# Performance work log

Hardware: AMD Instinct MI355X
Metric: run time of the kernel (lower is better)

The kernel has to match this reference:

```python
import jax, jax.numpy as jnp
import numpy as np

B, F, H, K, E = 512, 1280, 2560, 8, 9  # batch, feat_dim, 2*feat_dim, branching, n_internal
# Tree: root=node 0 (expert 0); level-1 nodes 1..8 (experts 1..8); level-2 leaves 9..72.

def setup_inputs() -> dict:
    key = jax.random.key(0)
    k0, k1, k2, k3, k4 = jax.random.split(key, 5)
    x = jax.random.normal(k0, (B, F), dtype=jnp.float32)
    W1 = jax.random.normal(k1, (E, F, H), dtype=jnp.float32) / np.sqrt(F)
    b1 = jnp.zeros((E, H), dtype=jnp.float32)
    W2 = jax.random.normal(k2, (E, H, K), dtype=jnp.float32) / np.sqrt(H)
    b2 = jnp.zeros((E, K), dtype=jnp.float32)
    return {"x": x, "W1": W1, "b1": b1, "W2": W2, "b2": b2}

def reference(x, W1, b1, W2, b2):
    # Batched experts: Linear(F->H) -> ReLU -> Linear(H->K), softmax over children.
    h = jax.nn.relu(jnp.einsum('bf,efh->ebh', x, W1) + b1[:, None, :])  # [E,B,H]
    logits = jnp.einsum('ebh,ehk->ebk', h, W2) + b2[:, None, :]          # [E,B,K]
    probs = jax.nn.softmax(logits, axis=-1)                              # [E,B,K]
    # Path products root->node for every node (matches leaf_probs in torch code).
    p0 = jnp.ones((1, x.shape[0]), dtype=x.dtype)        # root: prob 1        [1,B]
    p1 = probs[0].T                                       # nodes 1..8          [K,B]
    # leaves 9..72: parent of node n is 1+(n-9)//K, child index (n-9)%K
    p2 = (p1[:, None, :] * jnp.transpose(probs[1:E], (0, 2, 1))).reshape(K * K, -1)  # [64,B]
    leaf_probs = jnp.concatenate([p0, p1, p2], axis=0).T  # [B, 73]
    return leaf_probs, logits
```

## Files before the change

kernel.cpp:

```cpp
#include <hip/hip_runtime.h>

#define TB 512
#define TF 1280
#define TH 2560
#define TK 8
#define TE 9

typedef unsigned short ushortT;
typedef __attribute__((ext_vector_type(8))) short short8;
typedef __attribute__((ext_vector_type(4))) float floatx4;

__device__ __forceinline__ unsigned short f2bf(float f) {
  union { float f; unsigned u; } v; v.f = f;
  unsigned r = v.u + 0x7fffu + ((v.u >> 16) & 1u);
  return (unsigned short)(r >> 16);
}

__device__ __forceinline__ unsigned pk2(float a, float b) {
  union { float f; unsigned u; } ua, ub; ua.f = a; ub.f = b;
  unsigned ra = ua.u + 0x7fffu + ((ua.u >> 16) & 1u);
  unsigned rb = ub.u + 0x7fffu + ((ub.u >> 16) & 1u);
  return __builtin_amdgcn_perm(rb, ra, 0x07060302);
}

__device__ __forceinline__ void gl_lds16(const void* g, void* l) {
  __builtin_amdgcn_global_load_lds(
      (const __attribute__((address_space(1))) unsigned*)g,
      (__attribute__((address_space(3))) unsigned*)l, 16, 0, 0);
}

__global__ __launch_bounds__(256) void prepass(
    const float* __restrict__ x, const float* __restrict__ W2,
    ushortT* __restrict__ xb, ushortT* __restrict__ W2t) {
  const int i = blockIdx.x * 256 + threadIdx.x;
  if (i < TB * TF / 2) {
    float2 v = ((const float2*)x)[i];
    ((unsigned*)xb)[i] = pk2(v.x, v.y);
  } else {
    const int o = i - TB * TF / 2;
    if (o < TE * TK * TH) {
      const int hcol = o % TH;
      const int rest = o / TH;
      const int n = rest & 7;
      const int e = rest >> 3;
      W2t[(long)(e * TK + n) * TH + hcol] = f2bf(W2[((long)e * TH + hcol) * TK + n]);
    }
  }
}

__global__ __launch_bounds__(256, 3) void gemm1_relu(
    const ushortT* __restrict__ xb, const float* __restrict__ W1,
    const float* __restrict__ b1, ushortT* __restrict__ h) {
  __shared__ __align__(16) ushortT As[128 * 64];
  __shared__ __align__(16) ushortT Bs[128 * 72];

  const int t = threadIdx.x;
  const int tileN = blockIdx.x;
  const int e = tileN / 20;
  const int hbase = (tileN % 20) * 128;
  const int m0 = blockIdx.y * 128;

  const int lane = t & 63, w = t >> 6;
  const int wm = w & 1, wn = w >> 1;
  const int lm = lane & 15, lq = lane >> 4;

  const int kk4 = (t & 15) * 4;
  const int n0 = (t >> 4) * 8;

  floatx4 acc[4][4];
#pragma unroll
  for (int i = 0; i < 4; ++i)
#pragma unroll
    for (int j = 0; j < 4; ++j) acc[i][j] = (floatx4){0.f, 0.f, 0.f, 0.f};

  const float* wbase = W1 + ((long)e * TF) * TH + hbase + n0;

  floatx4 bv[4][2];
#pragma unroll
  for (int r = 0; r < 4; ++r)
#pragma unroll
    for (int c = 0; c < 2; ++c)
      bv[r][c] = *(const floatx4*)(wbase + (long)(kk4 + r) * TH + c * 4);

  for (int kt = 0; kt < TF / 64; ++kt) {
    const int k0 = kt * 64;
    if (kt) __syncthreads();

#pragma unroll
    for (int j = 0; j < 4; ++j) {
      const int s = j * 256 + w * 64 + lane;
      const int m = s >> 3;
      const int cc = (s & 7) ^ (m & 7);
      const ushortT* src = xb + (long)(m0 + m) * TF + k0 + cc * 8;
      gl_lds16(src, (void*)&As[(j * 256 + w * 64) * 8]);
    }
#pragma unroll
    for (int j = 0; j < 8; ++j) {
      const int c = j >> 2, q = j & 3;
      unsigned w0 = pk2(bv[0][c][q], bv[1][c][q]);
      unsigned w1 = pk2(bv[2][c][q], bv[3][c][q]);
      unsigned long long p = (unsigned long long)w0 | ((unsigned long long)w1 << 32);
      *(unsigned long long*)&Bs[(n0 + j) * 72 + kk4] = p;
    }
    __syncthreads();

    if (kt + 1 < TF / 64) {
#pragma unroll
      for (int r = 0; r < 4; ++r)
#pragma unroll
        for (int c = 0; c < 2; ++c)
          bv[r][c] = *(const floatx4*)(wbase + (long)(k0 + 64 + kk4 + r) * TH + c * 4);
    }

#pragma unroll
    for (int kk = 0; kk < 2; ++kk) {
      short8 af[4], bf[4];
#pragma unroll
      for (int mg = 0; mg < 4; ++mg) {
        const int m = wm * 64 + mg * 16 + lm;
        const int swz = (kk * 4 + lq) ^ (m & 7);
        af[mg] = *(const short8*)&As[m * 64 + swz * 8];
      }
#pragma unroll
      for (int ng = 0; ng < 4; ++ng) {
        const int n = wn * 64 + ng * 16 + lm;
        bf[ng] = *(const short8*)&Bs[n * 72 + kk * 32 + lq * 8];
      }
#pragma unroll
      for (int mg = 0; mg < 4; ++mg)
#pragma unroll
        for (int ng = 0; ng < 4; ++ng)
          acc[mg][ng] = __builtin_amdgcn_mfma_f32_16x16x32_bf16(af[mg], bf[ng], acc[mg][ng], 0, 0, 0);
    }
  }

#pragma unroll
  for (int mg = 0; mg < 4; ++mg) {
    const int row = m0 + wm * 64 + mg * 16 + lq * 4;
#pragma unroll
    for (int ng = 0; ng < 4; ++ng) {
      const int col = hbase + wn * 64 + ng * 16 + lm;
      const float bias = b1[e * TH + col];
      floatx4 c = acc[mg][ng];
#pragma unroll
      for (int r = 0; r < 4; ++r) {
        float v = c[r] + bias;
        v = v > 0.f ? v : 0.f;
        h[((long)e * TB + row + r) * TH + col] = f2bf(v);
      }
    }
  }
}

__global__ __launch_bounds__(256) void gemm2_softmax(
    const ushortT* __restrict__ h, const ushortT* __restrict__ W2t,
    const float* __restrict__ b2, float* __restrict__ logits_out,
    float* __restrict__ probs) {
  __shared__ float Ls[4][16][8];
  const int t = threadIdx.x;
  const int lane = t & 63, w = t >> 6;
  const int e = blockIdx.x >> 5;
  const int r0 = (blockIdx.x & 31) * 16;
  const int lm = lane & 15, lq = lane >> 4;

  const ushortT* hp = h + ((long)(e * TB + r0 + lm)) * TH + w * 640 + lq * 8;
  const int bn = lm < 8 ? lm : 7;
  const ushortT* wp = W2t + ((long)(e * TK + bn)) * TH + w * 640 + lq * 8;

  floatx4 acc = (floatx4){0.f, 0.f, 0.f, 0.f};
#pragma unroll
  for (int kt = 0; kt < 20; ++kt) {
    short8 a = *(const short8*)(hp + kt * 32);
    short8 b = *(const short8*)(wp + kt * 32);
    acc = __builtin_amdgcn_mfma_f32_16x16x32_bf16(a, b, acc, 0, 0, 0);
  }
  if (lm < 8) {
#pragma unroll
    for (int r = 0; r < 4; ++r) Ls[w][lq * 4 + r][lm] = acc[r];
  }
  __syncthreads();
  if (w == 0 && lm < 8) {
    const float bias = b2[e * TK + lm];
#pragma unroll
    for (int r = 0; r < 4; ++r) {
      const int row = lq * 4 + r;
      float v = Ls[0][row][lm] + Ls[1][row][lm] + Ls[2][row][lm] + Ls[3][row][lm] + bias;
      float mx = v;
      mx = fmaxf(mx, __shfl_xor(mx, 1, 64));
      mx = fmaxf(mx, __shfl_xor(mx, 2, 64));
      mx = fmaxf(mx, __shfl_xor(mx, 4, 64));
      float ex = __expf(v - mx);
      float sm = ex;
      sm += __shfl_xor(sm, 1, 64);
      sm += __shfl_xor(sm, 2, 64);
      sm += __shfl_xor(sm, 4, 64);
      const long idx = ((long)e * TB + r0 + row) * TK + lm;
      logits_out[idx] = v;
      probs[idx] = ex / sm;
    }
  }
}

__global__ __launch_bounds__(256) void leafk(const float* __restrict__ probs,
                                             float* __restrict__ out) {
  const int idx = blockIdx.x * 256 + threadIdx.x;
  if (idx >= TB * 73) return;
  const int b = idx / 73, c = idx % 73;
  float v;
  if (c == 0) {
    v = 1.0f;
  } else if (c < 9) {
    v = probs[(long)b * TK + (c - 1)];
  } else {
    const int i = (c - 9) >> 3, j = (c - 9) & 7;
    v = probs[(long)b * TK + i] * probs[((long)(1 + i) * TB + b) * TK + j];
  }
  out[idx] = v;
}

extern "C" void kernel_launch(void* const* d_in, const int* in_sizes, int n_in,
                              void* d_out, int out_size, void* d_ws, size_t ws_size,
                              hipStream_t stream) {
  const float* x  = (const float*)d_in[0];
  const float* W1 = (const float*)d_in[1];
  const float* b1 = (const float*)d_in[2];
  const float* W2 = (const float*)d_in[3];
  const float* b2 = (const float*)d_in[4];
  float* out = (float*)d_out;

  ushortT* h      = (ushortT*)d_ws;
  float*   probs  = (float*)((char*)d_ws + 23592960);
  ushortT* xb     = (ushortT*)((char*)d_ws + 23740416);
  ushortT* W2t    = (ushortT*)((char*)d_ws + 25051136);
  float* logits_out = out + TB * 73;

  prepass<<<2000, 256, 0, stream>>>(x, W2, xb, W2t);
  gemm1_relu<<<dim3(180, 4), 256, 0, stream>>>(xb, W1, b1, h);
  gemm2_softmax<<<TE * 32, 256, 0, stream>>>(h, W2t, b2, logits_out, probs);
  leafk<<<(TB * 73 + 255) / 256, 256, 0, stream>>>(probs, out);
}
```

Baseline: 245.2 us.

## Double-buffer W1 tile in LDS, load A fragments directly from global, remap grid

Rewrites the gemm1 main loop into a two-stage software pipeline, with two LDS buffers for the converted W1 tile and two register sets for the fp32 W1 prefetch. The x tile no longer goes through LDS: each wave loads its bf16 A fragments from global memory straight into registers, one k-step ahead. The grid becomes 1D with the four M tiles that share a W1 column tile placed on adjacent blocks, which should improve L2 reuse of W1, and launch bounds drop to 2 blocks per SM. The aim is fewer barriers and better overlap of global loads with MFMA, at the cost of higher register pressure, lower occupancy and uncoalesced, redundant global reads of A.

```diff
diff --git a/kernel.cpp b/kernel.cpp
--- a/kernel.cpp
+++ b/kernel.cpp
@@ -21,12 +21,6 @@
   unsigned ra = ua.u + 0x7fffu + ((ua.u >> 16) & 1u);
   unsigned rb = ub.u + 0x7fffu + ((ub.u >> 16) & 1u);
   return __builtin_amdgcn_perm(rb, ra, 0x07060302);
-}
-
-__device__ __forceinline__ void gl_lds16(const void* g, void* l) {
-  __builtin_amdgcn_global_load_lds(
-      (const __attribute__((address_space(1))) unsigned*)g,
-      (__attribute__((address_space(3))) unsigned*)l, 16, 0, 0);
 }
 
 __global__ __launch_bounds__(256) void prepass(
@@ -48,17 +42,18 @@
   }
 }
 
-__global__ __launch_bounds__(256, 3) void gemm1_relu(
+__global__ __launch_bounds__(256, 2) void gemm1_relu(
     const ushortT* __restrict__ xb, const float* __restrict__ W1,
     const float* __restrict__ b1, ushortT* __restrict__ h) {
-  __shared__ __align__(16) ushortT As[128 * 64];
-  __shared__ __align__(16) ushortT Bs[128 * 72];
+  __shared__ __align__(16) ushortT Bs[2][128 * 72];
 
   const int t = threadIdx.x;
-  const int tileN = blockIdx.x;
-  const int e = tileN / 20;
-  const int hbase = (tileN % 20) * 128;
-  const int m0 = blockIdx.y * 128;
+  const int bid = blockIdx.x;
+  const int ctile = bid >> 2;
+  const int mt = bid & 3;
+  const int e = ctile / 20;
+  const int hbase = (ctile % 20) * 128;
+  const int m0 = mt * 128;
 
   const int lane = t & 63, w = t >> 6;
   const int wm = w & 1, wn = w >> 1;
@@ -67,72 +62,82 @@
   const int kk4 = (t & 15) * 4;
   const int n0 = (t >> 4) * 8;
 
+  const float* wbase = W1 + ((long)e * TF) * TH + hbase + n0;
+  const ushortT* abase = xb + (long)(m0 + wm * 64 + lm) * TF + lq * 8;
+
   floatx4 acc[4][4];
 #pragma unroll
   for (int i = 0; i < 4; ++i)
 #pragma unroll
     for (int j = 0; j < 4; ++j) acc[i][j] = (floatx4){0.f, 0.f, 0.f, 0.f};
 
-  const float* wbase = W1 + ((long)e * TF) * TH + hbase + n0;
-
-  floatx4 bv[4][2];
-#pragma unroll
-  for (int r = 0; r < 4; ++r)
-#pragma unroll
-    for (int c = 0; c < 2; ++c)
-      bv[r][c] = *(const floatx4*)(wbase + (long)(kk4 + r) * TH + c * 4);
-
-  for (int kt = 0; kt < TF / 64; ++kt) {
-    const int k0 = kt * 64;
-    if (kt) __syncthreads();
-
-#pragma unroll
-    for (int j = 0; j < 4; ++j) {
-      const int s = j * 256 + w * 64 + lane;
-      const int m = s >> 3;
-      const int cc = (s & 7) ^ (m & 7);
-      const ushortT* src = xb + (long)(m0 + m) * TF + k0 + cc * 8;
-      gl_lds16(src, (void*)&As[(j * 256 + w * 64) * 8]);
-    }
+  floatx4 bva[4][2], bvb[4][2];
+  short8 afc[4][2], afn[4][2];
+
+  auto ldB = [&](floatx4 (&bv)[4][2], int kt) {
+    const float* p = wbase + (long)(kt * 64 + kk4) * TH;
+#pragma unroll
+    for (int r = 0; r < 4; ++r)
+#pragma unroll
+      for (int c = 0; c < 2; ++c)
+        bv[r][c] = *(const floatx4*)(p + (long)r * TH + c * 4);
+  };
+  auto wrB = [&](floatx4 (&bv)[4][2], int buf) {
 #pragma unroll
     for (int j = 0; j < 8; ++j) {
       const int c = j >> 2, q = j & 3;
       unsigned w0 = pk2(bv[0][c][q], bv[1][c][q]);
       unsigned w1 = pk2(bv[2][c][q], bv[3][c][q]);
       unsigned long long p = (unsigned long long)w0 | ((unsigned long long)w1 << 32);
-      *(unsigned long long*)&Bs[(n0 + j) * 72 + kk4] = p;
-    }
+      *(unsigned long long*)&Bs[buf][(n0 + j) * 72 + kk4] = p;
+    }
+  };
+  auto ldA = [&](short8 (&af)[4][2], int kt) {
+#pragma unroll
+    for (int mg = 0; mg < 4; ++mg)
+#pragma unroll
+      for (int kk = 0; kk < 2; ++kk)
+        af[mg][kk] = *(const short8*)(abase + (long)mg * 16 * TF + kt * 64 + kk * 32);
+  };
+  auto mma = [&](short8 (&af)[4][2], int buf) {
+#pragma unroll
+    for (int kk = 0; kk < 2; ++kk) {
+      short8 bf[4];
+#pragma unroll
+      for (int ng = 0; ng < 4; ++ng)
+        bf[ng] = *(const short8*)&Bs[buf][(wn * 64 + ng * 16 + lm) * 72 + kk * 32 + lq * 8];
+#pragma unroll
+      for (int mg = 0; mg < 4; ++mg)
+#pragma unroll
+        for (int ng = 0; ng < 4; ++ng)
+          acc[mg][ng] = __builtin_amdgcn_mfma_f32_16x16x32_bf16(af[mg][kk], bf[ng], acc[mg][ng], 0, 0, 0);
+    }
+  };
+
+  ldB(bva, 0);
+  ldB(bvb, 1);
+  ldA(afc, 0);
+  wrB(bva, 0);
+  __syncthreads();
+
+  for (int kt2 = 0; kt2 < 9; ++kt2) {
+    const int kt = 2 * kt2;
+    wrB(bvb, 1);
+    ldB(bva, kt + 2);
+    ldA(afn, kt + 1);
+    mma(afc, 0);
     __syncthreads();
-
-    if (kt + 1 < TF / 64) {
-#pragma unroll
-      for (int r = 0; r < 4; ++r)
-#pragma unroll
-        for (int c = 0; c < 2; ++c)
-          bv[r][c] = *(const floatx4*)(wbase + (long)(k0 + 64 + kk4 + r) * TH + c * 4);
-    }
-
-#pragma unroll
-    for (int kk = 0; kk < 2; ++kk) {
-      short8 af[4], bf[4];
-#pragma unroll
-      for (int mg = 0; mg < 4; ++mg) {
-        const int m = wm * 64 + mg * 16 + lm;
-        const int swz = (kk * 4 + lq) ^ (m & 7);
-        af[mg] = *(const short8*)&As[m * 64 + swz * 8];
-      }
-#pragma unroll
-      for (int ng = 0; ng < 4; ++ng) {
-        const int n = wn * 64 + ng * 16 + lm;
-        bf[ng] = *(const short8*)&Bs[n * 72 + kk * 32 + lq * 8];
-      }
-#pragma unroll
-      for (int mg = 0; mg < 4; ++mg)
-#pragma unroll
-        for (int ng = 0; ng < 4; ++ng)
-          acc[mg][ng] = __builtin_amdgcn_mfma_f32_16x16x32_bf16(af[mg], bf[ng], acc[mg][ng], 0, 0, 0);
-    }
-  }
+    wrB(bva, 0);
+    ldB(bvb, kt + 3);
+    ldA(afc, kt + 2);
+    mma(afn, 1);
+    __syncthreads();
+  }
+  wrB(bvb, 1);
+  ldA(afn, 19);
+  mma(afc, 0);
+  __syncthreads();
+  mma(afn, 1);
 
 #pragma unroll
   for (int mg = 0; mg < 4; ++mg) {
@@ -235,7 +240,7 @@
   float* logits_out = out + TB * 73;
 
   prepass<<<2000, 256, 0, stream>>>(x, W2, xb, W2t);
-  gemm1_relu<<<dim3(180, 4), 256, 0, stream>>>(xb, W1, b1, h);
+  gemm1_relu<<<720, 256, 0, stream>>>(xb, W1, b1, h);
   gemm2_softmax<<<TE * 32, 256, 0, stream>>>(h, W2t, b2, logits_out, probs);
   leafk<<<(TB * 73 + 255) / 256, 256, 0, stream>>>(probs, out);
 }
```

After: 283.0 us. 15.4% more time.

## Pre-pack W1 to bf16 and run LDS-free register double-buffered GEMM1

Applied to the files above, without the earlier changes.

Adds a pack pass that converts W1 from fp32 to bf16 in a k-interleaved layout that matches the MFMA B-operand fragments. GEMM1 is then rewritten to load A and B fragments straight from global memory into registers, double-buffered across k-tiles, with no LDS staging and no barriers. The aim is to take fp32-to-bf16 conversion and LDS synchronisation out of the GEMM inner loop. The cost is an extra full pass over W1 plus a large workspace write, and redundant global reads of A across waves. A simple LDS fallback kernel runs if the workspace is too small.

```diff
diff --git a/kernel.cpp b/kernel.cpp
--- a/kernel.cpp
+++ b/kernel.cpp
@@ -7,7 +7,9 @@
 #define TE 9
 
 typedef unsigned short ushortT;
+typedef unsigned long long u64;
 typedef __attribute__((ext_vector_type(8))) short short8;
+typedef __attribute__((ext_vector_type(4))) short short4v;
 typedef __attribute__((ext_vector_type(4))) float floatx4;
 
 __device__ __forceinline__ unsigned short f2bf(float f) {
@@ -21,12 +23,6 @@
   unsigned ra = ua.u + 0x7fffu + ((ua.u >> 16) & 1u);
   unsigned rb = ub.u + 0x7fffu + ((ub.u >> 16) & 1u);
   return __builtin_amdgcn_perm(rb, ra, 0x07060302);
-}
-
-__device__ __forceinline__ void gl_lds16(const void* g, void* l) {
-  __builtin_amdgcn_global_load_lds(
-      (const __attribute__((address_space(1))) unsigned*)g,
-      (__attribute__((address_space(3))) unsigned*)l, 16, 0, 0);
 }
 
 __global__ __launch_bounds__(256) void prepass(
@@ -48,92 +44,175 @@
   }
 }
 
-__global__ __launch_bounds__(256, 3) void gemm1_relu(
-    const ushortT* __restrict__ xb, const float* __restrict__ W1,
+__global__ __launch_bounds__(256) void pack_w1(const float* __restrict__ W1,
+                                               u64* __restrict__ W1p) {
+  const int bid = blockIdx.x;
+  const int nt = bid % 10;
+  const int kt = (bid / 10) % 80;
+  const int e  = bid / 800;
+  const int t = threadIdx.x;
+  const int tk = t >> 6, tc = t & 63;
+  const int k0 = kt * 16 + tk * 4;
+  const int n0 = nt * 256 + tc * 4;
+  const float* src = W1 + ((long)e * TF + k0) * TH + n0;
+  floatx4 v0 = *(const floatx4*)(src);
+  floatx4 v1 = *(const floatx4*)(src + TH);
+  floatx4 v2 = *(const floatx4*)(src + 2 * TH);
+  floatx4 v3 = *(const floatx4*)(src + 3 * TH);
+  u64 q[4];
+#pragma unroll
+  for (int i = 0; i < 4; ++i)
+    q[i] = (u64)pk2(v0[i], v1[i]) | ((u64)pk2(v2[i], v3[i]) << 32);
+  u64* dst = W1p + ((long)(e * 320 + (k0 >> 2)) * TH + n0);
+  *(ulonglong2*)(dst)     = make_ulonglong2(q[0], q[1]);
+  *(ulonglong2*)(dst + 2) = make_ulonglong2(q[2], q[3]);
+}
+
+__global__ __launch_bounds__(256) void gemm1_relu(
+    const ushortT* __restrict__ xb, const u64* __restrict__ W1p,
     const float* __restrict__ b1, ushortT* __restrict__ h) {
-  __shared__ __align__(16) ushortT As[128 * 64];
-  __shared__ __align__(16) ushortT Bs[128 * 72];
-
+  const int t = threadIdx.x;
+  const int lane = t & 63, w = t >> 6;
+  const int bid = blockIdx.x;
+  const int mt = bid & 7;
+  const int ctile = bid >> 3;
+  const int e = ctile / 10;
+  const int nt = ctile % 10;
+  const int m0 = mt * 64;
+  const int nb = nt * 256 + w * 64;
+  const int lm = lane & 15, lq = lane >> 4;
+
+  const ushortT* abase = xb + (long)(m0 + lm) * TF + lq * 8;
+  const u64* bbase = W1p + ((long)(e * 320 + lq * 2)) * TH + nb + lm;
+
+  floatx4 acc[4][4];
+#pragma unroll
+  for (int i = 0; i < 4; ++i)
+#pragma unroll
+    for (int j = 0; j < 4; ++j) acc[i][j] = (floatx4){0.f, 0.f, 0.f, 0.f};
+
+  short8 afc[4][2], afn[4][2];
+  u64 bfc[4][2][2], bfn[4][2][2];
+
+  auto ldA = [&](short8 (&af)[4][2], int kt) {
+#pragma unroll
+    for (int mg = 0; mg < 4; ++mg)
+#pragma unroll
+      for (int kk = 0; kk < 2; ++kk)
+        af[mg][kk] = *(const short8*)(abase + (long)mg * 16 * TF + kt * 64 + kk * 32);
+  };
+  auto ldB = [&](u64 (&bf)[4][2][2], int kt) {
+    const u64* p = bbase + (long)kt * 16 * TH;
+#pragma unroll
+    for (int ng = 0; ng < 4; ++ng)
+#pragma unroll
+      for (int kk = 0; kk < 2; ++kk) {
+        const u64* q = p + (long)kk * 8 * TH + ng * 16;
+        bf[ng][kk][0] = q[0];
+        bf[ng][kk][1] = q[TH];
+      }
+  };
+  auto mma = [&](short8 (&af)[4][2], u64 (&bf)[4][2][2]) {
+#pragma unroll
+    for (int kk = 0; kk < 2; ++kk)
+#pragma unroll
+      for (int ng = 0; ng < 4; ++ng) {
+        short8 b;
+        ((u64*)&b)[0] = bf[ng][kk][0];
+        ((u64*)&b)[1] = bf[ng][kk][1];
+#pragma unroll
+        for (int mg = 0; mg < 4; ++mg)
+          acc[mg][ng] = __builtin_amdgcn_mfma_f32_16x16x32_bf16(af[mg][kk], b, acc[mg][ng], 0, 0, 0);
+      }
+  };
+
+  ldA(afc, 0);
+  ldB(bfc, 0);
+  for (int kt = 0; kt < TF / 64 - 1; ++kt) {
+    if (kt & 1) { ldA(afc, kt + 1); ldB(bfc, kt + 1); mma(afn, bfn); }
+    else        { ldA(afn, kt + 1); ldB(bfn, kt + 1); mma(afc, bfc); }
+  }
+  mma(afn, bfn);
+
+#pragma unroll
+  for (int mg = 0; mg < 4; ++mg) {
+    const int row = m0 + mg * 16 + lq * 4;
+#pragma unroll
+    for (int ng = 0; ng < 4; ++ng) {
+      const int col = nb + ng * 16 + lm;
+      const float bias = b1[e * TH + col];
+      floatx4 c = acc[mg][ng];
+#pragma unroll
+      for (int r = 0; r < 4; ++r) {
+        float v = c[r] + bias;
+        v = v > 0.f ? v : 0.f;
+        h[((long)e * TB + row + r) * TH + col] = f2bf(v);
+      }
+    }
+  }
+}
+
+__global__ __launch_bounds__(256) void gemm1_fb(
+    const float* __restrict__ x, const float* __restrict__ W1,
+    const float* __restrict__ b1, ushortT* __restrict__ h) {
+  __shared__ __align__(16) ushortT As[128 * 40];
+  __shared__ __align__(16) ushortT Bs[128 * 40];
   const int t = threadIdx.x;
   const int tileN = blockIdx.x;
   const int e = tileN / 20;
   const int hbase = (tileN % 20) * 128;
   const int m0 = blockIdx.y * 128;
-
   const int lane = t & 63, w = t >> 6;
   const int wm = w & 1, wn = w >> 1;
   const int lm = lane & 15, lq = lane >> 4;
-
-  const int kk4 = (t & 15) * 4;
-  const int n0 = (t >> 4) * 8;
-
+  const int lk = lq * 8;
   floatx4 acc[4][4];
 #pragma unroll
   for (int i = 0; i < 4; ++i)
 #pragma unroll
     for (int j = 0; j < 4; ++j) acc[i][j] = (floatx4){0.f, 0.f, 0.f, 0.f};
-
-  const float* wbase = W1 + ((long)e * TF) * TH + hbase + n0;
-
-  floatx4 bv[4][2];
-#pragma unroll
-  for (int r = 0; r < 4; ++r)
-#pragma unroll
-    for (int c = 0; c < 2; ++c)
-      bv[r][c] = *(const floatx4*)(wbase + (long)(kk4 + r) * TH + c * 4);
-
-  for (int kt = 0; kt < TF / 64; ++kt) {
-    const int k0 = kt * 64;
+  const float* wp = W1 + (long)e * TF * TH + hbase;
+  const int cA = (t & 7) * 4;
+  const int mA = t >> 3;
+  const int nB = t & 127;
+  const int gB = t >> 7;
+  for (int kt = 0; kt < TF / 32; ++kt) {
+    const int k0 = kt * 32;
     if (kt) __syncthreads();
-
-#pragma unroll
-    for (int j = 0; j < 4; ++j) {
-      const int s = j * 256 + w * 64 + lane;
-      const int m = s >> 3;
-      const int cc = (s & 7) ^ (m & 7);
-      const ushortT* src = xb + (long)(m0 + m) * TF + k0 + cc * 8;
-      gl_lds16(src, (void*)&As[(j * 256 + w * 64) * 8]);
-    }
-#pragma unroll
-    for (int j = 0; j < 8; ++j) {
-      const int c = j >> 2, q = j & 3;
-      unsigned w0 = pk2(bv[0][c][q], bv[1][c][q]);
-      unsigned w1 = pk2(bv[2][c][q], bv[3][c][q]);
-      unsigned long long p = (unsigned long long)w0 | ((unsigned long long)w1 << 32);
-      *(unsigned long long*)&Bs[(n0 + j) * 72 + kk4] = p;
+#pragma unroll
+    for (int i = 0; i < 4; ++i) {
+      const int m = mA + 32 * i;
+      floatx4 v = *(const floatx4*)(x + (long)(m0 + m) * TF + k0 + cA);
+      short4v s; s.x = f2bf(v.x); s.y = f2bf(v.y); s.z = f2bf(v.z); s.w = f2bf(v.w);
+      *(short4v*)&As[m * 40 + cA] = s;
+    }
+    {
+      const float* bp = wp + (long)k0 * TH + nB;
+#pragma unroll
+      for (int q = 0; q < 4; ++q) {
+        const int k4 = gB * 16 + q * 4;
+        float f0 = bp[(long)(k4 + 0) * TH];
+        float f1 = bp[(long)(k4 + 1) * TH];
+        float f2 = bp[(long)(k4 + 2) * TH];
+        float f3 = bp[(long)(k4 + 3) * TH];
+        short4v s; s.x = f2bf(f0); s.y = f2bf(f1); s.z = f2bf(f2); s.w = f2bf(f3);
+        *(short4v*)&Bs[nB * 40 + k4] = s;
+      }
     }
     __syncthreads();
-
-    if (kt + 1 < TF / 64) {
-#pragma unroll
-      for (int r = 0; r < 4; ++r)
-#pragma unroll
-        for (int c = 0; c < 2; ++c)
-          bv[r][c] = *(const floatx4*)(wbase + (long)(k0 + 64 + kk4 + r) * TH + c * 4);
-    }
-
-#pragma unroll
-    for (int kk = 0; kk < 2; ++kk) {
-      short8 af[4], bf[4];
-#pragma unroll
-      for (int mg = 0; mg < 4; ++mg) {
-        const int m = wm * 64 + mg * 16 + lm;
-        const int swz = (kk * 4 + lq) ^ (m & 7);
-        af[mg] = *(const short8*)&As[m * 64 + swz * 8];
-      }
-#pragma unroll
-      for (int ng = 0; ng < 4; ++ng) {
-        const int n = wn * 64 + ng * 16 + lm;
-        bf[ng] = *(const short8*)&Bs[n * 72 + kk * 32 + lq * 8];
-      }
-#pragma unroll
-      for (int mg = 0; mg < 4; ++mg)
-#pragma unroll
-        for (int ng = 0; ng < 4; ++ng)
-          acc[mg][ng] = __builtin_amdgcn_mfma_f32_16x16x32_bf16(af[mg], bf[ng], acc[mg][ng], 0, 0, 0);
-    }
-  }
-
+    short8 af[4], bfr[4];
+#pragma unroll
+    for (int mg = 0; mg < 4; ++mg)
+      af[mg] = *(const short8*)&As[(wm * 64 + mg * 16 + lm) * 40 + lk];
+#pragma unroll
+    for (int ng = 0; ng < 4; ++ng)
+      bfr[ng] = *(const short8*)&Bs[(wn * 64 + ng * 16 + lm) * 40 + lk];
+#pragma unroll
+    for (int mg = 0; mg < 4; ++mg)
+#pragma unroll
+      for (int ng = 0; ng < 4; ++ng)
+        acc[mg][ng] = __builtin_amdgcn_mfma_f32_16x16x32_bf16(af[mg], bfr[ng], acc[mg][ng], 0, 0, 0);
+  }
 #pragma unroll
   for (int mg = 0; mg < 4; ++mg) {
     const int row = m0 + wm * 64 + mg * 16 + lq * 4;
@@ -228,14 +307,21 @@
   const float* b2 = (const float*)d_in[4];
   float* out = (float*)d_out;
 
-  ushortT* h      = (ushortT*)d_ws;
-  float*   probs  = (float*)((char*)d_ws + 23592960);
-  ushortT* xb     = (ushortT*)((char*)d_ws + 23740416);
-  ushortT* W2t    = (ushortT*)((char*)d_ws + 25051136);
+  ushortT* h     = (ushortT*)d_ws;
+  float*   probs = (float*)((char*)d_ws + 23592960);
+  ushortT* xb    = (ushortT*)((char*)d_ws + 23740416);
+  ushortT* W2t   = (ushortT*)((char*)d_ws + 25051136);
+  u64*     W1p   = (u64*)((char*)d_ws + 25419776);
+  const size_t NEED = 25419776 + 58982400;
   float* logits_out = out + TB * 73;
 
   prepass<<<2000, 256, 0, stream>>>(x, W2, xb, W2t);
-  gemm1_relu<<<dim3(180, 4), 256, 0, stream>>>(xb, W1, b1, h);
+  if (ws_size >= NEED) {
+    pack_w1<<<7200, 256, 0, stream>>>(W1, W1p);
+    gemm1_relu<<<720, 256, 0, stream>>>(xb, W1p, b1, h);
+  } else {
+    gemm1_fb<<<dim3(180, 4), 256, 0, stream>>>(x, W1, b1, h);
+  }
   gemm2_softmax<<<TE * 32, 256, 0, stream>>>(h, W2t, b2, logits_out, probs);
   leafk<<<(TB * 73 + 255) / 256, 256, 0, stream>>>(probs, out);
 }
```

Result: slower. 285.5 us (+16.4%).

## Fuse second GEMM into first GEMM epilogue with atomic logit accumulation

Applied to the files above, without the earlier changes.

The second small GEMM (H->K) now runs inside the first GEMM's epilogue. Each block stages its ReLU'd tile in LDS, multiplies it by the matching W2 slice and atomically adds partial logits into a zeroed buffer, so the large bf16 hidden activation is never written to or read back from global memory. The A operand is repacked into a k-quad-major layout and double-buffered, and W1 loads are reorganised. Softmax and leaf products are merged into one small kernel. This adds a memset, float atomics with nondeterministic summation order, and a 2-block final kernel with little parallelism.

```diff
diff --git a/kernel.cpp b/kernel.cpp
--- a/kernel.cpp
+++ b/kernel.cpp
@@ -7,6 +7,7 @@
 #define TE 9
 
 typedef unsigned short ushortT;
+typedef unsigned long long u64;
 typedef __attribute__((ext_vector_type(8))) short short8;
 typedef __attribute__((ext_vector_type(4))) float floatx4;
 
@@ -31,13 +32,14 @@
 
 __global__ __launch_bounds__(256) void prepass(
     const float* __restrict__ x, const float* __restrict__ W2,
-    ushortT* __restrict__ xb, ushortT* __restrict__ W2t) {
+    u64* __restrict__ xq, ushortT* __restrict__ W2t) {
   const int i = blockIdx.x * 256 + threadIdx.x;
-  if (i < TB * TF / 2) {
-    float2 v = ((const float2*)x)[i];
-    ((unsigned*)xb)[i] = pk2(v.x, v.y);
+  if (i < 320 * 512) {
+    const int kq = i >> 9, m = i & 511;
+    floatx4 v = *(const floatx4*)(x + (long)m * TF + kq * 4);
+    xq[i] = (u64)pk2(v.x, v.y) | ((u64)pk2(v.z, v.w) << 32);
   } else {
-    const int o = i - TB * TF / 2;
+    const int o = i - 320 * 512;
     if (o < TE * TK * TH) {
       const int hcol = o % TH;
       const int rest = o / TH;
@@ -48,24 +50,32 @@
   }
 }
 
-__global__ __launch_bounds__(256, 3) void gemm1_relu(
-    const ushortT* __restrict__ xb, const float* __restrict__ W1,
-    const float* __restrict__ b1, ushortT* __restrict__ h) {
-  __shared__ __align__(16) ushortT As[128 * 64];
-  __shared__ __align__(16) ushortT Bs[128 * 72];
+__global__ __launch_bounds__(256) void gemm1_fused(
+    const u64* __restrict__ xq, const float* __restrict__ W1,
+    const float* __restrict__ b1, const ushortT* __restrict__ W2t,
+    float* __restrict__ logacc) {
+  __shared__ __align__(16) char smem[34816];
+  u64* Aq0 = (u64*)smem;
+  u64* Aq1 = (u64*)(smem + 8448);
+  u64* Bq  = (u64*)(smem + 16896);
+  ushortT* Ht = (ushortT*)smem;
 
   const int t = threadIdx.x;
-  const int tileN = blockIdx.x;
-  const int e = tileN / 20;
-  const int hbase = (tileN % 20) * 128;
-  const int m0 = blockIdx.y * 128;
-
   const int lane = t & 63, w = t >> 6;
+  const int bid = blockIdx.x;
+  const int mt = bid & 3;
+  const int ctile = bid >> 2;
+  const int e = ctile / 20;
+  const int hbase = (ctile % 20) * 128;
+  const int m0 = mt * 128;
   const int wm = w & 1, wn = w >> 1;
   const int lm = lane & 15, lq = lane >> 4;
 
-  const int kk4 = (t & 15) * 4;
-  const int n0 = (t >> 4) * 8;
+  const int n4 = (t & 31) * 4;
+  const int kq = t >> 5;
+  const float* bgl = W1 + ((long)e * TF + kq * 4) * TH + hbase + n4;
+
+  const u64* agB = xq + m0 + lane * 2;
 
   floatx4 acc[4][4];
 #pragma unroll
@@ -73,149 +83,138 @@
 #pragma unroll
     for (int j = 0; j < 4; ++j) acc[i][j] = (floatx4){0.f, 0.f, 0.f, 0.f};
 
-  const float* wbase = W1 + ((long)e * TF) * TH + hbase + n0;
-
-  floatx4 bv[4][2];
-#pragma unroll
-  for (int r = 0; r < 4; ++r)
-#pragma unroll
-    for (int c = 0; c < 2; ++c)
-      bv[r][c] = *(const floatx4*)(wbase + (long)(kk4 + r) * TH + c * 4);
-
-  for (int kt = 0; kt < TF / 64; ++kt) {
-    const int k0 = kt * 64;
+  floatx4 bv[2][4];
+
+  auto ldB = [&](int buf, int kt) {
+#pragma unroll
+    for (int i = 0; i < 4; ++i)
+      bv[buf][i] = *(const floatx4*)(bgl + ((long)kt * 32 + i) * TH);
+  };
+  auto ldA = [&](u64* Adst, int kt) {
+    gl_lds16(agB + (long)(kt * 8 + w) * 512, &Adst[w * 132]);
+    gl_lds16(agB + (long)(kt * 8 + w + 4) * 512, &Adst[(w + 4) * 132]);
+  };
+
+  ldB(0, 0);
+  ldA(Aq0, 0);
+
+  for (int kt = 0; kt < 40; ++kt) {
+    const int c = kt & 1;
     if (kt) __syncthreads();
-
-#pragma unroll
-    for (int j = 0; j < 4; ++j) {
-      const int s = j * 256 + w * 64 + lane;
-      const int m = s >> 3;
-      const int cc = (s & 7) ^ (m & 7);
-      const ushortT* src = xb + (long)(m0 + m) * TF + k0 + cc * 8;
-      gl_lds16(src, (void*)&As[(j * 256 + w * 64) * 8]);
-    }
+    {
+      u64 q[4];
+#pragma unroll
+      for (int n = 0; n < 4; ++n)
+        q[n] = (u64)pk2(bv[c][0][n], bv[c][1][n]) |
+               ((u64)pk2(bv[c][2][n], bv[c][3][n]) << 32);
+      *(ulonglong2*)&Bq[kq * 132 + n4]     = make_ulonglong2(q[0], q[1]);
+      *(ulonglong2*)&Bq[kq * 132 + n4 + 2] = make_ulonglong2(q[2], q[3]);
+    }
+    __syncthreads();
+    if (kt < 39) {
+      ldB(c ^ 1, kt + 1);
+      ldA((kt & 1) ? Aq0 : Aq1, kt + 1);
+    }
+    const u64* Acur = (kt & 1) ? Aq1 : Aq0;
+
+    short8 af[4], bf[4];
+#pragma unroll
+    for (int mg = 0; mg < 4; ++mg) {
+      const int m = wm * 64 + mg * 16 + lm;
+      ((u64*)&af[mg])[0] = Acur[(2 * lq) * 132 + m];
+      ((u64*)&af[mg])[1] = Acur[(2 * lq + 1) * 132 + m];
+    }
+#pragma unroll
+    for (int ng = 0; ng < 4; ++ng) {
+      const int n = wn * 64 + ng * 16 + lm;
+      ((u64*)&bf[ng])[0] = Bq[(2 * lq) * 132 + n];
+      ((u64*)&bf[ng])[1] = Bq[(2 * lq + 1) * 132 + n];
+    }
+#pragma unroll
+    for (int mg = 0; mg < 4; ++mg)
+#pragma unroll
+      for (int ng = 0; ng < 4; ++ng)
+        acc[mg][ng] = __builtin_amdgcn_mfma_f32_16x16x32_bf16(af[mg], bf[ng], acc[mg][ng], 0, 0, 0);
+  }
+
+  float b1v[4];
+#pragma unroll
+  for (int ng = 0; ng < 4; ++ng)
+    b1v[ng] = b1[e * TH + hbase + wn * 64 + ng * 16 + lm];
+
+  __syncthreads();
+#pragma unroll
+  for (int mg = 0; mg < 4; ++mg) {
+    const int rbase = wm * 64 + mg * 16 + lq * 4;
+#pragma unroll
+    for (int ng = 0; ng < 4; ++ng) {
+      const int col = wn * 64 + ng * 16 + lm;
+      floatx4 cv = acc[mg][ng];
+#pragma unroll
+      for (int r = 0; r < 4; ++r) {
+        float v = cv[r] + b1v[ng];
+        v = v > 0.f ? v : 0.f;
+        Ht[(rbase + r) * 136 + col] = f2bf(v);
+      }
+    }
+  }
+  __syncthreads();
+
+#pragma unroll
+  for (int g = 0; g < 2; ++g) {
+    const int rgb = w * 32 + g * 16;
+    floatx4 d = (floatx4){0.f, 0.f, 0.f, 0.f};
+#pragma unroll
+    for (int kc = 0; kc < 4; ++kc) {
+      short8 a;
+      if (lm < 8)
+        a = *(const short8*)(W2t + ((long)(e * TK + lm)) * TH + hbase + kc * 32 + lq * 8);
+      else
+        a = (short8){0, 0, 0, 0, 0, 0, 0, 0};
+      short8 bfrag = *(const short8*)&Ht[(rgb + lm) * 136 + kc * 32 + lq * 8];
+      d = __builtin_amdgcn_mfma_f32_16x16x32_bf16(a, bfrag, d, 0, 0, 0);
+    }
+    if (lq < 2) {
+#pragma unroll
+      for (int r = 0; r < 4; ++r)
+        atomicAdd(&logacc[((long)e * TB + m0 + rgb + lm) * TK + lq * 4 + r], d[r]);
+    }
+  }
+}
+
+__global__ __launch_bounds__(256) void softmax_leaf(
+    const float* __restrict__ logacc, const float* __restrict__ b2,
+    float* __restrict__ out, float* __restrict__ logits_out) {
+  const int b = blockIdx.x * 256 + threadIdx.x;
+  if (b >= TB) return;
+  float p0[8];
+  out[(long)b * 73] = 1.0f;
+#pragma unroll
+  for (int e = 0; e < TE; ++e) {
+    float v[8], mx = -1e30f;
 #pragma unroll
     for (int j = 0; j < 8; ++j) {
-      const int c = j >> 2, q = j & 3;
-      unsigned w0 = pk2(bv[0][c][q], bv[1][c][q]);
-      unsigned w1 = pk2(bv[2][c][q], bv[3][c][q]);
-      unsigned long long p = (unsigned long long)w0 | ((unsigned long long)w1 << 32);
-      *(unsigned long long*)&Bs[(n0 + j) * 72 + kk4] = p;
-    }
-    __syncthreads();
-
-    if (kt + 1 < TF / 64) {
-#pragma unroll
-      for (int r = 0; r < 4; ++r)
-#pragma unroll
-        for (int c = 0; c < 2; ++c)
-          bv[r][c] = *(const floatx4*)(wbase + (long)(k0 + 64 + kk4 + r) * TH + c * 4);
-    }
-
-#pragma unroll
-    for (int kk = 0; kk < 2; ++kk) {
-      short8 af[4], bf[4];
-#pragma unroll
-      for (int mg = 0; mg < 4; ++mg) {
-        const int m = wm * 64 + mg * 16 + lm;
-        const int swz = (kk * 4 + lq) ^ (m & 7);
-        af[mg] = *(const short8*)&As[m * 64 + swz * 8];
+      v[j] = logacc[((long)e * TB + b) * TK + j] + b2[e * TK + j];
+      logits_out[((long)e * TB + b) * TK + j] = v[j];
+      mx = fmaxf(mx, v[j]);
+    }
+    float sm = 0.f;
+#pragma unroll
+    for (int j = 0; j < 8; ++j) { v[j] = __expf(v[j] - mx); sm += v[j]; }
+    const float inv = 1.0f / sm;
+    if (e == 0) {
+#pragma unroll
+      for (int j = 0; j < 8; ++j) {
+        p0[j] = v[j] * inv;
+        out[(long)b * 73 + 1 + j] = p0[j];
       }
-#pragma unroll
-      for (int ng = 0; ng < 4; ++ng) {
-        const int n = wn * 64 + ng * 16 + lm;
-        bf[ng] = *(const short8*)&Bs[n * 72 + kk * 32 + lq * 8];
-      }
-#pragma unroll
-      for (int mg = 0; mg < 4; ++mg)
-#pragma unroll
-        for (int ng = 0; ng < 4; ++ng)
-          acc[mg][ng] = __builtin_amdgcn_mfma_f32_16x16x32_bf16(af[mg], bf[ng], acc[mg][ng], 0, 0, 0);
-    }
-  }
-
-#pragma unroll
-  for (int mg = 0; mg < 4; ++mg) {
-    const int row = m0 + wm * 64 + mg * 16 + lq * 4;
-#pragma unroll
-    for (int ng = 0; ng < 4; ++ng) {
-      const int col = hbase + wn * 64 + ng * 16 + lm;
-      const float bias = b1[e * TH + col];
-      floatx4 c = acc[mg][ng];
-#pragma unroll
-      for (int r = 0; r < 4; ++r) {
-        float v = c[r] + bias;
-        v = v > 0.f ? v : 0.f;
-        h[((long)e * TB + row + r) * TH + col] = f2bf(v);
-      }
-    }
-  }
-}
-
-__global__ __launch_bounds__(256) void gemm2_softmax(
-    const ushortT* __restrict__ h, const ushortT* __restrict__ W2t,
-    const float* __restrict__ b2, float* __restrict__ logits_out,
-    float* __restrict__ probs) {
-  __shared__ float Ls[4][16][8];
-  const int t = threadIdx.x;
-  const int lane = t & 63, w = t >> 6;
-  const int e = blockIdx.x >> 5;
-  const int r0 = (blockIdx.x & 31) * 16;
-  const int lm = lane & 15, lq = lane >> 4;
-
-  const ushortT* hp = h + ((long)(e * TB + r0 + lm)) * TH + w * 640 + lq * 8;
-  const int bn = lm < 8 ? lm : 7;
-  const ushortT* wp = W2t + ((long)(e * TK + bn)) * TH + w * 640 + lq * 8;
-
-  floatx4 acc = (floatx4){0.f, 0.f, 0.f, 0.f};
-#pragma unroll
-  for (int kt = 0; kt < 20; ++kt) {
-    short8 a = *(const short8*)(hp + kt * 32);
-    short8 b = *(const short8*)(wp + kt * 32);
-    acc = __builtin_amdgcn_mfma_f32_16x16x32_bf16(a, b, acc, 0, 0, 0);
-  }
-  if (lm < 8) {
-#pragma unroll
-    for (int r = 0; r < 4; ++r) Ls[w][lq * 4 + r][lm] = acc[r];
-  }
-  __syncthreads();
-  if (w == 0 && lm < 8) {
-    const float bias = b2[e * TK + lm];
-#pragma unroll
-    for (int r = 0; r < 4; ++r) {
-      const int row = lq * 4 + r;
-      float v = Ls[0][row][lm] + Ls[1][row][lm] + Ls[2][row][lm] + Ls[3][row][lm] + bias;
-      float mx = v;
-      mx = fmaxf(mx, __shfl_xor(mx, 1, 64));
-      mx = fmaxf(mx, __shfl_xor(mx, 2, 64));
-      mx = fmaxf(mx, __shfl_xor(mx, 4, 64));
-      float ex = __expf(v - mx);
-      float sm = ex;
-      sm += __shfl_xor(sm, 1, 64);
-      sm += __shfl_xor(sm, 2, 64);
-      sm += __shfl_xor(sm, 4, 64);
-      const long idx = ((long)e * TB + r0 + row) * TK + lm;
-      logits_out[idx] = v;
-      probs[idx] = ex / sm;
-    }
-  }
-}
-
-__global__ __launch_bounds__(256) void leafk(const float* __restrict__ probs,
-                                             float* __restrict__ out) {
-  const int idx = blockIdx.x * 256 + threadIdx.x;
-  if (idx >= TB * 73) return;
-  const int b = idx / 73, c = idx % 73;
-  float v;
-  if (c == 0) {
-    v = 1.0f;
-  } else if (c < 9) {
-    v = probs[(long)b * TK + (c - 1)];
-  } else {
-    const int i = (c - 9) >> 3, j = (c - 9) & 7;
-    v = probs[(long)b * TK + i] * probs[((long)(1 + i) * TB + b) * TK + j];
-  }
-  out[idx] = v;
+    } else {
+      const float pp = p0[e - 1];
+#pragma unroll
+      for (int j = 0; j < 8; ++j)
+        out[(long)b * 73 + 9 + (e - 1) * 8 + j] = pp * v[j] * inv;
+    }
+  }
 }
 
 extern "C" void kernel_launch(void* const* d_in, const int* in_sizes, int n_in,
@@ -228,14 +227,13 @@
   const float* b2 = (const float*)d_in[4];
   float* out = (float*)d_out;
 
-  ushortT* h      = (ushortT*)d_ws;
-  float*   probs  = (float*)((char*)d_ws + 23592960);
-  ushortT* xb     = (ushortT*)((char*)d_ws + 23740416);
-  ushortT* W2t    = (ushortT*)((char*)d_ws + 25051136);
+  float*   logacc = (float*)d_ws;
+  u64*     xq     = (u64*)((char*)d_ws + 147456);
+  ushortT* W2t    = (ushortT*)((char*)d_ws + 1458176);
   float* logits_out = out + TB * 73;
 
-  prepass<<<2000, 256, 0, stream>>>(x, W2, xb, W2t);
-  gemm1_relu<<<dim3(180, 4), 256, 0, stream>>>(xb, W1, b1, h);
-  gemm2_softmax<<<TE * 32, 256, 0, stream>>>(h, W2t, b2, logits_out, probs);
-  leafk<<<(TB * 73 + 255) / 256, 256, 0, stream>>>(probs, out);
-}
+  hipMemsetAsync(logacc, 0, (size_t)TE * TB * TK * sizeof(float), stream);
+  prepass<<<1360, 256, 0, stream>>>(x, W2, xq, W2t);
+  gemm1_fused<<<720, 256, 0, stream>>>(xq, W1, b1, W2t, logacc);
+  softmax_leaf<<<2, 256, 0, stream>>>(logacc, b2, out, logits_out);
+}
```

New measurement: 287.0 us. 17.1% more time.
